# Kernel optimization log

Measured on AMD Instinct MI355X. Metric: run time of the kernel, lower is better.

## Reference

```python
import jax, jax.numpy as jnp
import numpy as np

NPOINT = 2048
NSAMPLE = 16
IN_CH = 64
OUT_CH = 128
LEAKY = 0.1
EPS = 1e-5


def leaky(x):
    return jnp.where(x >= 0, x, LEAKY * x)


def bn_train(x, g, b):
    # training-mode BatchNorm2d over (B, S, K) per channel; x: [B,C,S,K]
    m = jnp.mean(x, axis=(0, 2, 3), keepdims=True)
    v = jnp.var(x, axis=(0, 2, 3), keepdims=True)
    return (x - m) * jax.lax.rsqrt(v + EPS) * g.reshape(1, -1, 1, 1) + b.reshape(1, -1, 1, 1)


def fps(xyz, npoint):
    # furthest point sampling, xyz: [B,N,3], starts at index 0 (matches pointnet2)
    B, N, _ = xyz.shape
    def step(carry, _):
        dist, last = carry
        pt = jnp.take_along_axis(xyz, last[:, None, None], axis=1)  # [B,1,3]
        d = jnp.sum((xyz - pt) ** 2, axis=-1)                       # [B,N]
        dist = jnp.minimum(dist, d)
        nxt = jnp.argmax(dist, axis=-1).astype(jnp.int32)
        return (dist, nxt), nxt
    init = (jnp.full((B, N), 1e10, xyz.dtype), jnp.zeros((B,), jnp.int32))
    _, idxs = jax.lax.scan(step, init, None, length=npoint - 1)
    return jnp.concatenate([jnp.zeros((1, B), jnp.int32), idxs], axis=0).T  # [B,npoint]


def knn(nsample, xyz, new_xyz):
    # xyz: [B,N,3], new_xyz: [B,S,3] -> [B,S,nsample]
    sqr = (jnp.sum(new_xyz ** 2, -1)[:, :, None]
           + jnp.sum(xyz ** 2, -1)[:, None, :]
           - 2.0 * jnp.einsum('bsc,bnc->bsn', new_xyz, xyz))
    _, idx = jax.lax.top_k(-sqr, nsample)
    return idx


def gather_pts(points, idx):
    # points: [B,N,C], idx: [B,...] -> [B,...,C]
    return jax.vmap(lambda p, i: p[i])(points, idx)


def setup_inputs() -> dict:
    key = jax.random.key(0)
    ks = jax.random.split(key, 16)
    B, N = 4, 8192
    h = OUT_CH // 2
    sc = lambda fan: 1.0 / np.sqrt(fan)
    return {
        'xyz': jax.random.normal(ks[0], (B, 3, N), jnp.float32),
        'points': jax.random.normal(ks[1], (B, IN_CH, N), jnp.float32),
        'W0': jax.random.normal(ks[2], (IN_CH, h), jnp.float32) * sc(IN_CH),
        'b0': jnp.zeros((h,), jnp.float32),
        'g0': jnp.ones((h,), jnp.float32),
        'be0': jnp.zeros((h,), jnp.float32),
        'W1': jax.random.normal(ks[3], (9, h), jnp.float32) * sc(9),
        'b1': jnp.zeros((h,), jnp.float32),
        'g1': jnp.ones((h,), jnp.float32),
        'be1': jnp.zeros((h,), jnp.float32),
        'Ws': jax.random.normal(ks[4], (OUT_CH, OUT_CH), jnp.float32) * sc(OUT_CH),
        'W2': jax.random.normal(ks[5], (OUT_CH, OUT_CH), jnp.float32) * sc(OUT_CH),
        'b2': jnp.zeros((OUT_CH,), jnp.float32),
        'g2': jnp.ones((OUT_CH,), jnp.float32),
        'be2': jnp.zeros((OUT_CH,), jnp.float32),
    }


def reference(xyz, points, W0, b0, g0, be0, W1, b1, g1, be1, Ws, W2, b2, g2, be2):
    B = xyz.shape[0]
    xyz_t = jnp.transpose(xyz, (0, 2, 1))      # [B,N,3]
    pts_t = jnp.transpose(points, (0, 2, 1))   # [B,N,D]

    fps_idx = fps(xyz_t, NPOINT)               # [B,S]
    new_xyz = gather_pts(xyz_t, fps_idx)       # [B,S,3]
    idx = knn(NSAMPLE, xyz_t, new_xyz)         # [B,S,K]

    grouped_xyz = gather_pts(xyz_t, idx)                      # [B,S,K,3]
    grouped_xyz_norm = grouped_xyz - new_xyz[:, :, None, :]   # [B,S,K,3]
    grouped_points = gather_pts(pts_t, idx)                   # [B,S,K,D]

    # mlp0: 1x1 conv + BN + leaky  -> [B,h,S,K]
    new_points = leaky(bn_train(
        jnp.einsum('bskd,dc->bcsk', grouped_points, W0) + b0.reshape(1, -1, 1, 1), g0, be0))

    extended = jnp.broadcast_to(jnp.transpose(new_xyz, (0, 2, 1))[..., None],
                                (B, 3, NPOINT, NSAMPLE))
    concat = jnp.concatenate([extended,
                              jnp.transpose(grouped_xyz, (0, 3, 1, 2)),
                              jnp.transpose(grouped_xyz_norm, (0, 3, 1, 2))], axis=1)  # [B,9,S,K]

    lse_part = leaky(bn_train(
        jnp.einsum('bcsk,cd->bdsk', concat, W1) + b1.reshape(1, -1, 1, 1), g1, be1))
    lse1 = jnp.concatenate([lse_part, new_points], axis=1)    # [B,out,S,K]

    # score_fn1: 1x1 conv (no bias) -> leaky -> softmax over nsample
    scores = jax.nn.softmax(leaky(jnp.einsum('bcsk,cd->bdsk', lse1, Ws)), axis=-1)
    features1 = jnp.sum(scores * lse1, axis=-1, keepdims=True)  # [B,out,S,1]

    new_points_out = leaky(bn_train(
        jnp.einsum('bcsk,cd->bdsk', features1, W2) + b2.reshape(1, -1, 1, 1), g2, be2))
    new_points_out = jnp.squeeze(new_points_out, -1)            # [B,out,S]

    return jnp.transpose(new_xyz, (0, 2, 1)), new_points_out, fps_idx
```

## Files before the change

kernel.cpp:

```cpp
#include <hip/hip_runtime.h>

#define BB 4
#define NN 8192
#define SS 2048
#define KK 16
#define INCH 64
#define HH 64
#define OUTC 128
#define LEAKY_A 0.1f
#define EPSF 1e-5f

__device__ __forceinline__ float sq3(float a, float b, float c) {
    return __fadd_rn(__fadd_rn(__fmul_rn(a, a), __fmul_rn(b, b)), __fmul_rn(c, c));
}

__device__ __forceinline__ float leaky_f(float x) { return x >= 0.f ? x : LEAKY_A * x; }

__device__ __forceinline__ int spread3(int v) {
    return (v & 1) | ((v & 2) << 2) | ((v & 4) << 4);
}

__device__ __forceinline__ unsigned long long shfl_xor_u64(unsigned long long v, int off) {
    unsigned lo = (unsigned)v, hi = (unsigned)(v >> 32);
    lo = __shfl_xor(lo, off);
    hi = __shfl_xor(hi, off);
    return ((unsigned long long)hi << 32) | lo;
}

__global__ __launch_bounds__(1024)
void fps_kernel(const float* __restrict__ xyz,
                float* __restrict__ new_xyz,
                float* __restrict__ out0,
                float* __restrict__ out2)
{
    int b = blockIdx.x, t = threadIdx.x;
    int lane = t & 63, wid = t >> 6;
    const float* xb = xyz + (long)b * 3 * NN;

    __shared__ unsigned short perm[NN];
    __shared__ unsigned int hist[512];
    __shared__ unsigned int starts[512];
    __shared__ unsigned int wsum[8];
    __shared__ float wred[16][6];
    __shared__ unsigned long long skey[2][16];
    __shared__ float4 sval[2][16];
    __shared__ unsigned short pick[SS];

    float lx[8], ly[8], lz[8];
    float mnx = 3.4e38f, mny = 3.4e38f, mnz = 3.4e38f;
    float mxx = -3.4e38f, mxy = -3.4e38f, mxz = -3.4e38f;
#pragma unroll
    for (int j = 0; j < 8; ++j) {
        int n = t * 8 + j;
        lx[j] = xb[n]; ly[j] = xb[NN + n]; lz[j] = xb[2 * NN + n];
        mnx = fminf(mnx, lx[j]); mxx = fmaxf(mxx, lx[j]);
        mny = fminf(mny, ly[j]); mxy = fmaxf(mxy, ly[j]);
        mnz = fminf(mnz, lz[j]); mxz = fmaxf(mxz, lz[j]);
    }
#pragma unroll
    for (int off = 1; off < 64; off <<= 1) {
        mnx = fminf(mnx, __shfl_xor(mnx, off)); mxx = fmaxf(mxx, __shfl_xor(mxx, off));
        mny = fminf(mny, __shfl_xor(mny, off)); mxy = fmaxf(mxy, __shfl_xor(mxy, off));
        mnz = fminf(mnz, __shfl_xor(mnz, off)); mxz = fmaxf(mxz, __shfl_xor(mxz, off));
    }
    if (lane == 0) {
        wred[wid][0] = mnx; wred[wid][1] = mny; wred[wid][2] = mnz;
        wred[wid][3] = mxx; wred[wid][4] = mxy; wred[wid][5] = mxz;
    }
    if (t < 512) hist[t] = 0;
    __syncthreads();
    mnx = wred[0][0]; mny = wred[0][1]; mnz = wred[0][2];
    mxx = wred[0][3]; mxy = wred[0][4]; mxz = wred[0][5];
#pragma unroll
    for (int w = 1; w < 16; ++w) {
        mnx = fminf(mnx, wred[w][0]); mny = fminf(mny, wred[w][1]); mnz = fminf(mnz, wred[w][2]);
        mxx = fmaxf(mxx, wred[w][3]); mxy = fmaxf(mxy, wred[w][4]); mxz = fmaxf(mxz, wred[w][5]);
    }
    float sclx = 8.0f / fmaxf(mxx - mnx, 1e-9f);
    float scly = 8.0f / fmaxf(mxy - mny, 1e-9f);
    float sclz = 8.0f / fmaxf(mxz - mnz, 1e-9f);
    int mcode[8];
#pragma unroll
    for (int j = 0; j < 8; ++j) {
        int ux = (int)((lx[j] - mnx) * sclx); ux = ux < 0 ? 0 : (ux > 7 ? 7 : ux);
        int uy = (int)((ly[j] - mny) * scly); uy = uy < 0 ? 0 : (uy > 7 ? 7 : uy);
        int uz = (int)((lz[j] - mnz) * sclz); uz = uz < 0 ? 0 : (uz > 7 ? 7 : uz);
        mcode[j] = spread3(ux) | (spread3(uy) << 1) | (spread3(uz) << 2);
        atomicAdd(&hist[mcode[j]], 1u);
    }
    __syncthreads();
    unsigned v = 0, incl = 0;
    if (t < 512) {
        v = hist[t];
        incl = v;
#pragma unroll
        for (int d = 1; d < 64; d <<= 1) {
            unsigned u = __shfl_up(incl, d);
            if (lane >= d) incl += u;
        }
        if (lane == 63) wsum[wid] = incl;
    }
    __syncthreads();
    if (t < 512) {
        unsigned off = 0;
        for (int w = 0; w < wid; ++w) off += wsum[w];
        starts[t] = off + incl - v;
    }
    __syncthreads();
#pragma unroll
    for (int j = 0; j < 8; ++j) {
        unsigned pos = atomicAdd(&starts[mcode[j]], 1u);
        perm[pos] = (unsigned short)(t * 8 + j);
    }
    __syncthreads();

    float px[8], py[8], pz[8], dist[8];
    int oi[8];
#pragma unroll
    for (int j = 0; j < 8; ++j) {
        int o = perm[t * 8 + j];
        oi[j] = o;
        px[j] = xb[o]; py[j] = xb[NN + o]; pz[j] = xb[2 * NN + o];
        dist[j] = 1e10f;
    }
#define CSWAP(a, b) { if (oi[a] > oi[b]) { int ti = oi[a]; oi[a] = oi[b]; oi[b] = ti; \
    float tf; tf = px[a]; px[a] = px[b]; px[b] = tf; \
    tf = py[a]; py[a] = py[b]; py[b] = tf; \
    tf = pz[a]; pz[a] = pz[b]; pz[b] = tf; } }
    CSWAP(0,1) CSWAP(2,3) CSWAP(4,5) CSWAP(6,7)
    CSWAP(0,2) CSWAP(1,3) CSWAP(4,6) CSWAP(5,7)
    CSWAP(1,2) CSWAP(5,6)
    CSWAP(0,4) CSWAP(1,5) CSWAP(2,6) CSWAP(3,7)
    CSWAP(2,4) CSWAP(3,5)
    CSWAP(1,2) CSWAP(3,4) CSWAP(5,6)
#undef CSWAP
    float tbx0 = 3.4e38f, tby0 = 3.4e38f, tbz0 = 3.4e38f;
    float tbx1 = -3.4e38f, tby1 = -3.4e38f, tbz1 = -3.4e38f;
#pragma unroll
    for (int j = 0; j < 8; ++j) {
        tbx0 = fminf(tbx0, px[j]); tbx1 = fmaxf(tbx1, px[j]);
        tby0 = fminf(tby0, py[j]); tby1 = fmaxf(tby1, py[j]);
        tbz0 = fminf(tbz0, pz[j]); tbz1 = fmaxf(tbz1, pz[j]);
    }

    unsigned kh = __float_as_uint(1e10f), kl = 0u;
    float bx = 0.f, by = 0.f, bz = 0.f;
    bool iswin = false;

    if (t == 0) pick[0] = 0;
    float cx = xb[0], cy = xb[NN], cz = xb[2 * NN];

#define DPPMAX(m, CTRL) { \
    unsigned _o = (unsigned)__builtin_amdgcn_update_dpp(0, (int)(m), CTRL, 0xf, 0xf, true); \
    (m) = (_o > (m)) ? _o : (m); \
}

    for (int i = 1; i < SS; ++i) {
        float gx = fmaxf(fmaxf(tbx0 - cx, cx - tbx1), 0.f);
        float gy = fmaxf(fmaxf(tby0 - cy, cy - tby1), 0.f);
        float gz = fmaxf(fmaxf(tbz0 - cz, cz - tbz1), 0.f);
        float lb = gx * gx + gy * gy + gz * gz;
        bool thr_act = lb <= __uint_as_float(kh) * 1.00001f;
        if (__any((int)thr_act)) {
            if (thr_act) {
                float bv = -1.f; int bi = 0; float nbx = 0.f, nby = 0.f, nbz = 0.f;
#pragma unroll
                for (int j = 0; j < 8; ++j) {
                    float dx = __fsub_rn(px[j], cx), dy = __fsub_rn(py[j], cy), dz = __fsub_rn(pz[j], cz);
                    float d = sq3(dx, dy, dz);
                    float nd = fminf(dist[j], d);
                    dist[j] = nd;
                    if (nd > bv) { bv = nd; bi = oi[j]; nbx = px[j]; nby = py[j]; nbz = pz[j]; }
                }
                kh = __float_as_uint(bv); kl = ~(unsigned)bi;
                bx = nbx; by = nby; bz = nbz;
            }
            unsigned m = kh;
            DPPMAX(m, 0x111) DPPMAX(m, 0x112) DPPMAX(m, 0x114)
            DPPMAX(m, 0x118) DPPMAX(m, 0x142) DPPMAX(m, 0x143)
            unsigned wmax = (unsigned)__builtin_amdgcn_readlane((int)m, 63);
            unsigned long long mask = __ballot((int)(kh == wmax));
            int wlane;
            if (__popcll(mask) == 1) {
                wlane = (int)__builtin_ctzll(mask);
            } else {
                unsigned t2 = (kh == wmax) ? kl : 0u;
                DPPMAX(t2, 0x111) DPPMAX(t2, 0x112) DPPMAX(t2, 0x114)
                DPPMAX(t2, 0x118) DPPMAX(t2, 0x142) DPPMAX(t2, 0x143)
                unsigned klm = (unsigned)__builtin_amdgcn_readlane((int)t2, 63);
                wlane = (int)__builtin_ctzll(__ballot((int)(kh == wmax && kl == klm)));
            }
            iswin = (lane == wlane);
        }
        int buf = i & 1;
        if (iswin) {
            skey[buf][wid] = ((unsigned long long)kh << 32) | kl;
            sval[buf][wid] = make_float4(bx, by, bz, 0.f);
        }
        __syncthreads();
        unsigned long long sk = skey[buf][lane & 15];
        float4 sv = sval[buf][lane & 15];
        unsigned xh = (unsigned)(sk >> 32), xl = (unsigned)sk;
        unsigned m2 = xh;
        DPPMAX(m2, 0x111) DPPMAX(m2, 0x112) DPPMAX(m2, 0x114) DPPMAX(m2, 0x118)
        unsigned wh = (unsigned)__builtin_amdgcn_readlane((int)m2, 15);
        unsigned long long mk = __ballot((int)(lane < 16 && xh == wh));
        int widx;
        if (__popcll(mk) == 1) {
            widx = (int)__builtin_ctzll(mk);
        } else {
            unsigned t3 = (lane < 16 && xh == wh) ? xl : 0u;
            DPPMAX(t3, 0x111) DPPMAX(t3, 0x112) DPPMAX(t3, 0x114) DPPMAX(t3, 0x118)
            unsigned wl2 = (unsigned)__builtin_amdgcn_readlane((int)t3, 15);
            widx = (int)__builtin_ctzll(__ballot((int)(lane < 16 && xh == wh && xl == wl2)));
        }
        cx = __shfl(sv.x, widx);
        cy = __shfl(sv.y, widx);
        cz = __shfl(sv.z, widx);
        unsigned wl = (unsigned)__shfl((int)xl, widx);
        if (t == 0) pick[i] = (unsigned short)(~wl);
    }
#undef DPPMAX
    __syncthreads();
    for (int i = t; i < SS; i += 1024) {
        int n = pick[i];
        float x = xb[n], y = xb[NN + n], z = xb[2 * NN + n];
        new_xyz[((long)b * SS + i) * 3 + 0] = x;
        new_xyz[((long)b * SS + i) * 3 + 1] = y;
        new_xyz[((long)b * SS + i) * 3 + 2] = z;
        out0[(long)b * 3 * SS + 0 * SS + i] = x;
        out0[(long)b * 3 * SS + 1 * SS + i] = y;
        out0[(long)b * 3 * SS + 2 * SS + i] = z;
        out2[b * SS + i] = (float)n;
    }
}

__global__ __launch_bounds__(256)
void knn_kernel(const float* __restrict__ xyz,
                const float* __restrict__ new_xyz,
                int* __restrict__ knn_idx,
                const float* __restrict__ points,
                const float* __restrict__ W0, const float* __restrict__ b0,
                const float* __restrict__ W1, const float* __restrict__ b1,
                float* __restrict__ sums)
{
    int gwave = (blockIdx.x * 256 + threadIdx.x) >> 6;
    int lane = threadIdx.x & 63;
    int wid = threadIdx.x >> 6;
    int b = gwave / SS;
    const float* xb = xyz + (long)b * 3 * NN;
    float nx = new_xyz[(long)gwave * 3 + 0];
    float ny = new_xyz[(long)gwave * 3 + 1];
    float nz = new_xyz[(long)gwave * 3 + 2];
    float snew = sq3(nx, ny, nz);
    unsigned long long kk[16];
    const unsigned long long KINIT = 0xFF7FFFFF7FFFFFFFull;
#pragma unroll
    for (int j = 0; j < 16; ++j) kk[j] = KINIT;
    unsigned long long wk = KINIT; int ws = 0;
    for (int tix = 0; tix < NN / 64; ++tix) {
        int n = tix * 64 + lane;
        float qx = xb[n], qy = xb[NN + n], qz = xb[2 * NN + n];
        float sx = sq3(qx, qy, qz);
        float dot = __fadd_rn(__fadd_rn(__fmul_rn(nx, qx), __fmul_rn(ny, qy)), __fmul_rn(nz, qz));
        float d = __fsub_rn(__fadd_rn(snew, sx), __fmul_rn(2.0f, dot));
        unsigned ud = __float_as_uint(d);
        ud = ((int)ud < 0) ? ~ud : (ud | 0x80000000u);
        unsigned long long key = ((unsigned long long)ud << 32) | (unsigned)n;
        if (key < wk) {
            kk[ws] = key;
            wk = kk[0]; ws = 0;
#pragma unroll
            for (int j = 1; j < 16; ++j) {
                bool g = kk[j] > wk;
                wk = g ? kk[j] : wk; ws = g ? j : ws;
            }
        }
    }
    int myres = 0;
#pragma unroll
    for (int r = 0; r < 16; ++r) {
        unsigned long long mn = kk[0]; int ms = 0;
#pragma unroll
        for (int j = 1; j < 16; ++j) {
            bool l = kk[j] < mn;
            mn = l ? kk[j] : mn; ms = l ? j : ms;
        }
        unsigned long long bm = mn;
#pragma unroll
        for (int off = 1; off < 64; off <<= 1) {
            unsigned long long om = shfl_xor_u64(bm, off);
            if (om < bm) bm = om;
        }
        if (mn == bm) kk[ms] = 0xFFFFFFFFFFFFFFFFull;
        if (lane == r) myres = (int)(unsigned)(bm & 0xffffffffull);
    }
    if (lane < 16) knn_idx[(long)gwave * 16 + lane] = myres;

    const float* pb = points + (long)b * INCH * NN + (long)lane * NN;
    float a0 = 0, q0 = 0, a1 = 0, q1 = 0;
#pragma unroll
    for (int k = 0; k < 16; ++k) {
        int n = __shfl(myres, k);
        float gp = pb[n];
        float x0 = b0[lane];
#pragma unroll
        for (int d = 0; d < 64; ++d)
            x0 = fmaf(__shfl(gp, d), W0[d * 64 + lane], x0);
        float qx = xb[n], qy = xb[NN + n], qz = xb[2 * NN + n];
        float c9[9] = {nx, ny, nz, qx, qy, qz, qx - nx, qy - ny, qz - nz};
        float x1 = b1[lane];
#pragma unroll
        for (int j = 0; j < 9; ++j) x1 = fmaf(c9[j], W1[j * 64 + lane], x1);
        a0 += x0; q0 += x0 * x0; a1 += x1; q1 += x1 * x1;
    }
    __shared__ float red[4][4][64];
    red[0][wid][lane] = a0; red[1][wid][lane] = q0; red[2][wid][lane] = a1; red[3][wid][lane] = q1;
    __syncthreads();
    if (threadIdx.x < 64) {
#pragma unroll
        for (int arr = 0; arr < 4; ++arr) {
            float v = red[arr][0][lane] + red[arr][1][lane] + red[arr][2][lane] + red[arr][3][lane];
            atomicAdd(&sums[arr * 64 + lane], v);
        }
    }
}

__global__ __launch_bounds__(256)
void center_kernel(const float* __restrict__ points, const float* __restrict__ xyz,
                   const float* __restrict__ new_xyz, const int* __restrict__ knn_idx,
                   const float* __restrict__ W0, const float* __restrict__ b0,
                   const float* __restrict__ W1, const float* __restrict__ b1,
                   const float* __restrict__ sums01,
                   const float* __restrict__ g0, const float* __restrict__ be0,
                   const float* __restrict__ g1, const float* __restrict__ be1,
                   const float* __restrict__ Ws,
                   float* __restrict__ features1)
{
    int xcd = blockIdx.x & 7;
    int b = xcd >> 1;
    int s = ((blockIdx.x >> 3) << 1) + (xcd & 1);
    int bs = (b << 11) + s;
    int wid = threadIdx.x >> 6, lane = threadIdx.x & 63;
    __shared__ float lse[KK][OUTC];
    __shared__ float sraw[KK][OUTC];
    __shared__ float ssl[4][64];
    if (threadIdx.x < 64) {
        int c = threadIdx.x;
        float inv = 1.0f / (float)(BB * SS * KK);
        float m0 = sums01[c] * inv,        v0 = sums01[64 + c] * inv - m0 * m0;
        float m1 = sums01[128 + c] * inv,  v1 = sums01[192 + c] * inv - m1 * m1;
        float s0 = g0[c] / sqrtf(v0 + EPSF);
        float s1 = g1[c] / sqrtf(v1 + EPSF);
        ssl[0][c] = s0; ssl[1][c] = be0[c] - m0 * s0;
        ssl[2][c] = s1; ssl[3][c] = be1[c] - m1 * s1;
    }
    __syncthreads();
    float sc0 = ssl[0][lane], sh0 = ssl[1][lane], sc1 = ssl[2][lane], sh1 = ssl[3][lane];
    float nx = new_xyz[(long)bs * 3], ny = new_xyz[(long)bs * 3 + 1], nz = new_xyz[(long)bs * 3 + 2];
    const float* xb = xyz + (long)b * 3 * NN;
    const float* pb = points + (long)b * INCH * NN + (long)lane * NN;
    int n4[4]; float gp4[4];
#pragma unroll
    for (int kk = 0; kk < 4; ++kk) n4[kk] = knn_idx[(long)bs * 16 + wid * 4 + kk];
#pragma unroll
    for (int kk = 0; kk < 4; ++kk) gp4[kk] = pb[n4[kk]];
#pragma unroll
    for (int kk = 0; kk < 4; ++kk) {
        int k = wid * 4 + kk;
        int n = n4[kk];
        float gp = gp4[kk];
        float x0 = b0[lane];
#pragma unroll
        for (int d = 0; d < 64; ++d)
            x0 = fmaf(__shfl(gp, d), W0[d * 64 + lane], x0);
        float qx = xb[n], qy = xb[NN + n], qz = xb[2 * NN + n];
        float c9[9] = {nx, ny, nz, qx, qy, qz, qx - nx, qy - ny, qz - nz};
        float x1 = b1[lane];
#pragma unroll
        for (int j = 0; j < 9; ++j) x1 = fmaf(c9[j], W1[j * 64 + lane], x1);
        x0 = leaky_f(x0 * sc0 + sh0);
        x1 = leaky_f(x1 * sc1 + sh1);
        lse[k][lane] = x1;
        lse[k][64 + lane] = x0;
    }
    __syncthreads();
    int d = threadIdx.x & 127;
    int kg = threadIdx.x >> 7;
    float acc[8];
#pragma unroll
    for (int i = 0; i < 8; ++i) acc[i] = 0.f;
    for (int c = 0; c < OUTC; ++c) {
        float w = Ws[c * OUTC + d];
#pragma unroll
        for (int i = 0; i < 8; ++i) acc[i] = fmaf(lse[kg * 8 + i][c], w, acc[i]);
    }
#pragma unroll
    for (int i = 0; i < 8; ++i) sraw[kg * 8 + i][d] = leaky_f(acc[i]);
    __syncthreads();
    if (threadIdx.x < OUTC) {
        int dd = threadIdx.x;
        float vals[KK];
        float mx = -3.4e38f;
#pragma unroll
        for (int k = 0; k < KK; ++k) { vals[k] = sraw[k][dd]; mx = fmaxf(mx, vals[k]); }
        float sum = 0.f;
#pragma unroll
        for (int k = 0; k < KK; ++k) { vals[k] = __expf(vals[k] - mx); sum += vals[k]; }
        float invs = 1.0f / sum;
        float feat = 0.f;
#pragma unroll
        for (int k = 0; k < KK; ++k) feat = fmaf(vals[k] * invs, lse[k][dd], feat);
        features1[(long)bs * OUTC + dd] = feat;
    }
}

__global__ __launch_bounds__(256)
void mlp2_kernel(const float* __restrict__ features1,
                 const float* __restrict__ W2, const float* __restrict__ b2,
                 float* __restrict__ x2,
                 float* __restrict__ sums2)
{
    int p0 = blockIdx.x * 16;
    __shared__ float f[16][OUTC];
    for (int i = threadIdx.x; i < 16 * OUTC; i += 256)
        f[i >> 7][i & 127] = features1[(long)p0 * OUTC + i];
    __syncthreads();
    int d = threadIdx.x & 127;
    int g = threadIdx.x >> 7;
    float acc[8];
#pragma unroll
    for (int i = 0; i < 8; ++i) acc[i] = b2[d];
    for (int c = 0; c < OUTC; ++c) {
        float w = W2[c * OUTC + d];
#pragma unroll
        for (int i = 0; i < 8; ++i) acc[i] = fmaf(f[g * 8 + i][c], w, acc[i]);
    }
    float s = 0.f, q = 0.f;
#pragma unroll
    for (int i = 0; i < 8; ++i) {
        x2[(long)(p0 + g * 8 + i) * OUTC + d] = acc[i];
        s += acc[i]; q += acc[i] * acc[i];
    }
    __shared__ float rs[2][2][OUTC];
    rs[0][g][d] = s; rs[1][g][d] = q;
    __syncthreads();
    if (threadIdx.x < OUTC) {
        atomicAdd(&sums2[d],        rs[0][0][d] + rs[0][1][d]);
        atomicAdd(&sums2[OUTC + d], rs[1][0][d] + rs[1][1][d]);
    }
}

__global__ __launch_bounds__(256)
void out1_kernel(const float* __restrict__ x2, const float* __restrict__ sums2,
                 const float* __restrict__ g2, const float* __restrict__ be2,
                 float* __restrict__ out1)
{
    int bc = blockIdx.x;
    int b = bc >> 7, c = bc & 127;
    float inv = 1.0f / (float)(BB * SS);
    float m = sums2[c] * inv, v = sums2[OUTC + c] * inv - m * m;
    float sc = g2[c] / sqrtf(v + EPSF);
    float sh = be2[c] - m * sc;
    for (int s = threadIdx.x; s < SS; s += 256) {
        float val = x2[((long)(b * SS + s)) * OUTC + c] * sc + sh;
        out1[(long)b * OUTC * SS + (long)c * SS + s] = leaky_f(val);
    }
}

extern "C" void kernel_launch(void* const* d_in, const int* in_sizes, int n_in,
                              void* d_out, int out_size, void* d_ws, size_t ws_size,
                              hipStream_t stream)
{
    const float* xyz    = (const float*)d_in[0];
    const float* points = (const float*)d_in[1];
    const float* W0  = (const float*)d_in[2];
    const float* b0  = (const float*)d_in[3];
    const float* g0  = (const float*)d_in[4];
    const float* be0 = (const float*)d_in[5];
    const float* W1  = (const float*)d_in[6];
    const float* b1  = (const float*)d_in[7];
    const float* g1  = (const float*)d_in[8];
    const float* be1 = (const float*)d_in[9];
    const float* Ws  = (const float*)d_in[10];
    const float* W2  = (const float*)d_in[11];
    const float* b2  = (const float*)d_in[12];
    const float* g2  = (const float*)d_in[13];
    const float* be2 = (const float*)d_in[14];

    char* ws = (char*)d_ws;
    float* nxyz   = (float*)(ws + 32768);
    int*   knn_i  = (int*)(ws + 131072);
    float* sums01 = (float*)(ws + 655360);
    float* sums2  = (float*)(ws + 656384);
    float* feat1  = (float*)(ws + 659456);
    float* x2     = (float*)(ws + 659456 + 4194304);

    float* out0 = (float*)d_out;
    float* out1 = out0 + (long)BB * 3 * SS;
    float* out2 = out1 + (long)BB * OUTC * SS;

    hipMemsetAsync(sums01, 0, 2048, stream);

    fps_kernel<<<BB, 1024, 0, stream>>>(xyz, nxyz, out0, out2);
    knn_kernel<<<(BB * SS) / 4, 256, 0, stream>>>(xyz, nxyz, knn_i, points, W0, b0, W1, b1, sums01);
    center_kernel<<<BB * SS, 256, 0, stream>>>(points, xyz, nxyz, knn_i, W0, b0, W1, b1,
                                               sums01, g0, be0, g1, be1, Ws, feat1);
    mlp2_kernel<<<(BB * SS) / 16, 256, 0, stream>>>(feat1, W2, b2, x2, sums2);
    out1_kernel<<<BB * OUTC, 256, 0, stream>>>(x2, sums2, g2, be2, out1);
}
```

Before: 2.418 ms.

## Trim FPS cross-wave reduction loads, remap KNN blocks per XCD, prefetch gathers

In the FPS loop, the winning key's high word is packed into the float4 value slot, so the 64-bit key read from shared memory is only needed on ties or by thread 0. This shortens the serial per-iteration critical path. The KNN kernel remaps block indices so each pair of XCDs handles one batch, aiming to keep that batch's xyz and points in the local L2. All 16 gathered point loads are also issued before the FMA loop so their latency overlaps, at the cost of more registers.

After: 2.443 ms. No clear change (+1.0%).

```diff
diff --git a/kernel.cpp b/kernel.cpp
--- a/kernel.cpp
+++ b/kernel.cpp
@@ -195,30 +195,33 @@
         int buf = i & 1;
         if (iswin) {
             skey[buf][wid] = ((unsigned long long)kh << 32) | kl;
-            sval[buf][wid] = make_float4(bx, by, bz, 0.f);
+            sval[buf][wid] = make_float4(bx, by, bz, __uint_as_float(kh));
         }
         __syncthreads();
-        unsigned long long sk = skey[buf][lane & 15];
         float4 sv = sval[buf][lane & 15];
-        unsigned xh = (unsigned)(sk >> 32), xl = (unsigned)sk;
-        unsigned m2 = xh;
+        unsigned mh = __float_as_uint(sv.w);
+        unsigned m2 = mh;
         DPPMAX(m2, 0x111) DPPMAX(m2, 0x112) DPPMAX(m2, 0x114) DPPMAX(m2, 0x118)
         unsigned wh = (unsigned)__builtin_amdgcn_readlane((int)m2, 15);
-        unsigned long long mk = __ballot((int)(lane < 16 && xh == wh));
+        unsigned long long mk = __ballot((int)(lane < 16 && mh == wh));
         int widx;
         if (__popcll(mk) == 1) {
             widx = (int)__builtin_ctzll(mk);
         } else {
-            unsigned t3 = (lane < 16 && xh == wh) ? xl : 0u;
+            unsigned long long sk = skey[buf][lane & 15];
+            unsigned xl = (unsigned)sk;
+            unsigned t3 = (lane < 16 && mh == wh) ? xl : 0u;
             DPPMAX(t3, 0x111) DPPMAX(t3, 0x112) DPPMAX(t3, 0x114) DPPMAX(t3, 0x118)
             unsigned wl2 = (unsigned)__builtin_amdgcn_readlane((int)t3, 15);
-            widx = (int)__builtin_ctzll(__ballot((int)(lane < 16 && xh == wh && xl == wl2)));
+            widx = (int)__builtin_ctzll(__ballot((int)(lane < 16 && mh == wh && xl == wl2)));
         }
         cx = __shfl(sv.x, widx);
         cy = __shfl(sv.y, widx);
         cz = __shfl(sv.z, widx);
-        unsigned wl = (unsigned)__shfl((int)xl, widx);
-        if (t == 0) pick[i] = (unsigned short)(~wl);
+        if (t == 0) {
+            unsigned wl = (unsigned)(skey[buf][widx] & 0xffffffffull);
+            pick[i] = (unsigned short)(~wl);
+        }
     }
 #undef DPPMAX
     __syncthreads();
@@ -244,10 +247,12 @@
                 const float* __restrict__ W1, const float* __restrict__ b1,
                 float* __restrict__ sums)
 {
-    int gwave = (blockIdx.x * 256 + threadIdx.x) >> 6;
     int lane = threadIdx.x & 63;
     int wid = threadIdx.x >> 6;
-    int b = gwave / SS;
+    int xcd = blockIdx.x & 7;
+    int b = xcd >> 1;
+    int idx_in_b = ((blockIdx.x >> 3) << 1) + (xcd & 1);
+    int gwave = b * SS + idx_in_b * 4 + wid;
     const float* xb = xyz + (long)b * 3 * NN;
     float nx = new_xyz[(long)gwave * 3 + 0];
     float ny = new_xyz[(long)gwave * 3 + 1];
@@ -298,11 +303,17 @@
     if (lane < 16) knn_idx[(long)gwave * 16 + lane] = myres;
 
     const float* pb = points + (long)b * INCH * NN + (long)lane * NN;
+    int ns[16];
+#pragma unroll
+    for (int k = 0; k < 16; ++k) ns[k] = __shfl(myres, k);
+    float gps[16];
+#pragma unroll
+    for (int k = 0; k < 16; ++k) gps[k] = pb[ns[k]];
     float a0 = 0, q0 = 0, a1 = 0, q1 = 0;
 #pragma unroll
     for (int k = 0; k < 16; ++k) {
-        int n = __shfl(myres, k);
-        float gp = pb[n];
+        int n = ns[k];
+        float gp = gps[k];
         float x0 = b0[lane];
 #pragma unroll
         for (int d = 0; d < 64; ++d)
```
